# Performance work log

Hardware: AMD Instinct MI355X
Metric: run time of the kernel (lower is better)

## Reference

```python
import jax, jax.numpy as jnp
import numpy as np

NUM_HEADS = 16
WINDOW = 128  # local-attention half-width used by the mask generator
NEG_INF = -1e9


def setup_inputs() -> dict:
    key = jax.random.key(0)
    ks = jax.random.split(key, 12)
    T, N, C = 2048, 2, 1024
    s = 1.0 / np.sqrt(C)
    inp = {
        "q": jax.random.normal(ks[0], (T, N, C), jnp.float32),
        "k": jax.random.normal(ks[1], (T, N, C), jnp.float32),
        "v": jax.random.normal(ks[2], (T, N, C), jnp.float32),
        # MultiHeadDispatch: separate q/k/v input projections + output projection (with bias)
        "Wq": jax.random.normal(ks[3], (C, C), jnp.float32) * s,
        "bq": jnp.zeros((C,), jnp.float32),
        "Wk": jax.random.normal(ks[4], (C, C), jnp.float32) * s,
        "bk": jnp.zeros((C,), jnp.float32),
        "Wv": jax.random.normal(ks[5], (C, C), jnp.float32) * s,
        "bv": jnp.zeros((C,), jnp.float32),
        "Wo": jax.random.normal(ks[6], (C, C), jnp.float32) * s,
        "bo": jnp.zeros((C,), jnp.float32),
        "key_length": jax.random.randint(ks[7], (N,), 1, T, dtype=jnp.int32),
    }
    return inp


def _build_mask(Lq, Lk, key_length):
    # mask_generator: banded local-window mask, True = attend
    i = jnp.arange(Lq)[:, None]
    j = jnp.arange(Lk)[None, :]
    local = jnp.abs(i - j) <= WINDOW                      # (Lq, Lk)
    # forward(): mask[i, :, :key_length[i]] = 1  -> unmask prefix keys per batch elem
    prefix = j[None, :, :] < key_length[:, None, None]    # (N, Lq, Lk)
    return local[None, :, :] | prefix                     # (N, Lq, Lk) bool


def reference(q, k, v, Wq, bq, Wk, bk, Wv, bv, Wo, bo, key_length):
    T, N, C = q.shape
    H = NUM_HEADS
    Dh = C // H
    mask = _build_mask(q.shape[0], k.shape[0], key_length)  # (N, Lq, Lk)

    def heads(x, W, b):
        # (T, N, C) -> project -> (N, H, T, Dh)
        y = x @ W.T + b
        return jnp.transpose(y.reshape(x.shape[0], N, H, Dh), (1, 2, 0, 3))

    qh = heads(q, Wq, bq)
    kh = heads(k, Wk, bk)
    vh = heads(v, Wv, bv)

    scale = 1.0 / np.sqrt(Dh).astype(np.float32)
    scores = jnp.einsum('nhqd,nhkd->nhqk', qh, kh) * scale  # (N, H, Lq, Lk)
    scores = jnp.where(mask[:, None, :, :], scores, NEG_INF)
    att = jax.nn.softmax(scores, axis=-1)
    y = jnp.einsum('nhqk,nhkd->nhqd', att, vh)              # (N, H, Lq, Dh)
    y = jnp.transpose(y, (2, 0, 1, 3)).reshape(T, N, C)     # back to (t, n, c)
    return y @ Wo.T + bo
```

## Files before the change

### kernel.cpp

```cpp
#include <hip/hip_runtime.h>
#include <math.h>

#define T_DIM 2048
#define N_B   2
#define C_DIM 1024
#define H_DIM 16
#define DH    64
#define M_DIM 4096
#define WIN   128

typedef _Float16 h8 __attribute__((ext_vector_type(8)));
typedef float    f4 __attribute__((ext_vector_type(4)));

#if __has_builtin(__builtin_amdgcn_exp2f)
#define EXP2(x) __builtin_amdgcn_exp2f(x)
#else
#define EXP2(x) __expf((x) * 0.693147180559945f)
#endif

__device__ __forceinline__ void glds16(const _Float16* g, _Float16* l) {
    typedef const __attribute__((address_space(1))) unsigned int guint;
    typedef __attribute__((address_space(3))) unsigned int luint;
    __builtin_amdgcn_global_load_lds((guint*)g, (luint*)l, 16, 0, 0);
}

struct CvtA { const float* s; _Float16* d; int n; };
struct Cvt7 { CvtA a[7]; };

__global__ __launch_bounds__(256) void cvt_k(Cvt7 c) {
    CvtA A = c.a[blockIdx.y];
    const int i = (blockIdx.x * 256 + threadIdx.x) * 8;
    if (i >= A.n) return;
    const float4 v0 = *(const float4*)&A.s[i];
    const float4 v1 = *(const float4*)&A.s[i + 4];
    h8 o;
    o[0] = (_Float16)v0.x; o[1] = (_Float16)v0.y;
    o[2] = (_Float16)v0.z; o[3] = (_Float16)v0.w;
    o[4] = (_Float16)v1.x; o[5] = (_Float16)v1.y;
    o[6] = (_Float16)v1.z; o[7] = (_Float16)v1.w;
    *(h8*)&A.d[i] = o;
}

struct QkvArgs {
    const _Float16* x[3];
    const _Float16* w[3];
    const float*    b[3];
    _Float16*       out[3];
};

__global__ __launch_bounds__(256) void proj_qkv(QkvArgs args) {
    const int z = blockIdx.z;
    const _Float16* __restrict__ A = args.x[z];
    const _Float16* __restrict__ B = args.w[z];
    const float* __restrict__ bias = args.b[z];
    _Float16* __restrict__ out     = args.out[z];

    __shared__ _Float16 Asm[3][128 * 32];
    __shared__ _Float16 Bsm[3][128 * 32];
    const int tid  = threadIdx.x;
    const int lane = tid & 63;
    const int wave = tid >> 6;
    const int wr = wave >> 1, wc = wave & 1;
    const int l15 = lane & 15, hi = lane >> 4;
    const int m0 = blockIdx.x << 7;
    const int o0 = blockIdx.y << 7;

    auto STAGE = [&](int b, int k0) {
#pragma unroll
        for (int c = 0; c < 2; ++c) {
            const int chunk = tid + c * 256;
            const int row = chunk >> 2, c4 = chunk & 3;
            const int sc = (c4 ^ ((row >> 1) & 3)) << 3;
            glds16(&A[(size_t)(m0 + row) * C_DIM + k0 + sc], &Asm[b][chunk << 3]);
            glds16(&B[(size_t)(o0 + row) * C_DIM + k0 + sc], &Bsm[b][chunk << 3]);
        }
    };

    f4 acc[4][4];
    const f4 z4 = {0.f, 0.f, 0.f, 0.f};
#pragma unroll
    for (int i = 0; i < 4; ++i)
#pragma unroll
        for (int j = 0; j < 4; ++j) acc[i][j] = z4;

    STAGE(0, 0);
    STAGE(1, 32);
    int buf = 0;
    for (int k0 = 0; k0 < C_DIM; k0 += 32) {
        if (k0 + 32 < C_DIM) {
            asm volatile("s_waitcnt vmcnt(4)" ::: "memory");
        } else {
            asm volatile("s_waitcnt vmcnt(0)" ::: "memory");
        }
        __builtin_amdgcn_s_barrier();
        __builtin_amdgcn_sched_barrier(0);
        if (k0 + 64 < C_DIM) {
            const int nb = (buf + 2 >= 3) ? buf - 1 : buf + 2;
            STAGE(nb, k0 + 64);
        }

        h8 a[4], b[4];
#pragma unroll
        for (int mr = 0; mr < 4; ++mr) {
            const int R = wr * 64 + mr * 16 + l15;
            a[mr] = *(const h8*)&Asm[buf][R * 32 + ((hi ^ ((R >> 1) & 3)) << 3)];
        }
#pragma unroll
        for (int nf = 0; nf < 4; ++nf) {
            const int R = wc * 64 + nf * 16 + l15;
            b[nf] = *(const h8*)&Bsm[buf][R * 32 + ((hi ^ ((R >> 1) & 3)) << 3)];
        }
#pragma unroll
        for (int mr = 0; mr < 4; ++mr)
#pragma unroll
            for (int nf = 0; nf < 4; ++nf)
                acc[mr][nf] = __builtin_amdgcn_mfma_f32_16x16x32_f16(
                    a[mr], b[nf], acc[mr][nf], 0, 0, 0);

        buf = (buf + 1 >= 3) ? 0 : buf + 1;
    }

#pragma unroll
    for (int nf = 0; nf < 4; ++nf) {
        const int o = o0 + wc * 64 + nf * 16 + l15;
        const float bb = bias[o];
        const int hh = o >> 6, d = o & 63;
#pragma unroll
        for (int mr = 0; mr < 4; ++mr)
#pragma unroll
            for (int reg = 0; reg < 4; ++reg) {
                const int m = m0 + wr * 64 + mr * 16 + 4 * hi + reg;
                const float val = acc[mr][nf][reg] + bb;
                const int t = m >> 1, n = m & 1;
                if (z == 2) {
                    out[(((size_t)(n * H_DIM + hh)) * DH + d) * T_DIM + t] = (_Float16)val;
                } else {
                    out[(((size_t)(n * H_DIM + hh)) * T_DIM + t) * DH + d] = (_Float16)val;
                }
            }
    }
}

__global__ __launch_bounds__(256) void proj_o(
    const _Float16* __restrict__ A, const _Float16* __restrict__ B,
    const float* __restrict__ bias, float* __restrict__ out)
{
    __shared__ _Float16 Asm[3][128 * 32];
    __shared__ _Float16 Bsm[3][128 * 32];
    const int tid  = threadIdx.x;
    const int lane = tid & 63;
    const int wave = tid >> 6;
    const int wr = wave >> 1, wc = wave & 1;
    const int l15 = lane & 15, hi = lane >> 4;
    const int m0 = blockIdx.x << 7;
    const int o0 = blockIdx.y << 7;

    auto STAGE = [&](int b, int k0) {
#pragma unroll
        for (int c = 0; c < 2; ++c) {
            const int chunk = tid + c * 256;
            const int row = chunk >> 2, c4 = chunk & 3;
            const int sc = (c4 ^ ((row >> 1) & 3)) << 3;
            glds16(&A[(size_t)(m0 + row) * C_DIM + k0 + sc], &Asm[b][chunk << 3]);
            glds16(&B[(size_t)(o0 + row) * C_DIM + k0 + sc], &Bsm[b][chunk << 3]);
        }
    };

    f4 acc[4][4];
    const f4 z4 = {0.f, 0.f, 0.f, 0.f};
#pragma unroll
    for (int i = 0; i < 4; ++i)
#pragma unroll
        for (int j = 0; j < 4; ++j) acc[i][j] = z4;

    STAGE(0, 0);
    STAGE(1, 32);
    int buf = 0;
    for (int k0 = 0; k0 < C_DIM; k0 += 32) {
        if (k0 + 32 < C_DIM) {
            asm volatile("s_waitcnt vmcnt(4)" ::: "memory");
        } else {
            asm volatile("s_waitcnt vmcnt(0)" ::: "memory");
        }
        __builtin_amdgcn_s_barrier();
        __builtin_amdgcn_sched_barrier(0);
        if (k0 + 64 < C_DIM) {
            const int nb = (buf + 2 >= 3) ? buf - 1 : buf + 2;
            STAGE(nb, k0 + 64);
        }

        h8 a[4], b[4];
#pragma unroll
        for (int mr = 0; mr < 4; ++mr) {
            const int R = wr * 64 + mr * 16 + l15;
            a[mr] = *(const h8*)&Asm[buf][R * 32 + ((hi ^ ((R >> 1) & 3)) << 3)];
        }
#pragma unroll
        for (int nf = 0; nf < 4; ++nf) {
            const int R = wc * 64 + nf * 16 + l15;
            b[nf] = *(const h8*)&Bsm[buf][R * 32 + ((hi ^ ((R >> 1) & 3)) << 3)];
        }
#pragma unroll
        for (int mr = 0; mr < 4; ++mr)
#pragma unroll
            for (int nf = 0; nf < 4; ++nf)
                acc[mr][nf] = __builtin_amdgcn_mfma_f32_16x16x32_f16(
                    a[mr], b[nf], acc[mr][nf], 0, 0, 0);

        buf = (buf + 1 >= 3) ? 0 : buf + 1;
    }

#pragma unroll
    for (int nf = 0; nf < 4; ++nf) {
        const int o = o0 + wc * 64 + nf * 16 + l15;
        const float bb = bias[o];
#pragma unroll
        for (int mr = 0; mr < 4; ++mr)
#pragma unroll
            for (int reg = 0; reg < 4; ++reg) {
                const int m = m0 + wr * 64 + mr * 16 + 4 * hi + reg;
                out[(size_t)m * C_DIM + o] = acc[mr][nf][reg] + bb;
            }
    }
}

__global__ __launch_bounds__(256, 2) void attn_v7(
    const _Float16* __restrict__ QH, const _Float16* __restrict__ KH,
    const _Float16* __restrict__ VT, const int* __restrict__ key_length,
    _Float16* __restrict__ Y)
{
    __shared__ _Float16 Ks[2][64 * 64];
    __shared__ _Float16 Vs[2][64 * 64];
    __shared__ _Float16 Ps[4][32 * 72];

    const int nh = blockIdx.x;
    const int n  = nh >> 4;
    const int h  = nh & 15;
    const int qb = blockIdx.y << 7;
    const int kl = key_length[n];
    const int tid  = threadIdx.x;
    const int wave = tid >> 6;
    const int lane = tid & 63;
    const int l15 = lane & 15, hi = lane >> 4;
    const int qw = qb + wave * 32;
    const int swz = l15 & 7;

    const size_t hb = (size_t)nh * T_DIM * DH;
    const _Float16* Qb = QH + hb;
    const _Float16* Kb = KH + hb;
    const _Float16* Vb = VT + hb;

    const int klc0 = ((kl + 63) >> 6) << 6;
    const int klc  = (klc0 < T_DIM) ? klc0 : T_DIM;
    const int blo  = (qb >= WIN) ? ((qb - WIN) & ~63) : 0;
    int bhi = ((qb + 127 + WIN) >> 6) << 6;
    if (bhi > T_DIM - 64) bhi = T_DIM - 64;
    auto nxt = [&](int k0) -> int {
        k0 += 64;
        if (k0 < klc) return k0;
        if (k0 < blo) k0 = blo;
        return (k0 <= bhi) ? k0 : -1;
    };

    auto STAGE = [&](int b, int k0) {
#pragma unroll
        for (int c = 0; c < 2; ++c) {
            const int slot = wave * 128 + c * 64 + lane;
            const int r = slot >> 3, c16 = slot & 7;
            const int sc = (c16 ^ (r & 7)) << 3;
            glds16(&Kb[(size_t)(k0 + r) * DH + sc], &Ks[b][slot << 3]);
        }
#pragma unroll
        for (int c = 0; c < 2; ++c) {
            const int slot = wave * 128 + c * 64 + lane;
            const int r = slot >> 3, c16 = slot & 7;
            const int sc = (c16 ^ (r & 7)) << 3;
            glds16(&Vb[(size_t)r * T_DIM + k0 + sc], &Vs[b][slot << 3]);
        }
    };

    h8 qa[2][2];
#pragma unroll
    for (int mr = 0; mr < 2; ++mr)
#pragma unroll
        for (int ks = 0; ks < 2; ++ks)
            qa[mr][ks] = *(const h8*)&Qb[(size_t)(qw + mr * 16 + l15) * DH + ks * 32 + hi * 8];

    f4 O[2][4];
    const f4 z4 = {0.f, 0.f, 0.f, 0.f};
#pragma unroll
    for (int mr = 0; mr < 2; ++mr)
#pragma unroll
        for (int df = 0; df < 4; ++df) O[mr][df] = z4;
    float m_i[2][4], lp[2][4];
#pragma unroll
    for (int mr = 0; mr < 2; ++mr)
#pragma unroll
        for (int r = 0; r < 4; ++r) { m_i[mr][r] = -1e30f; lp[mr][r] = 0.f; }

    const float SC = 0.18033688f;

    auto TILE = [&](int b, int k0) {
        h8 kb[2][4];
#pragma unroll
        for (int ks = 0; ks < 2; ++ks)
#pragma unroll
            for (int cf = 0; cf < 4; ++cf)
                kb[ks][cf] = *(const h8*)&Ks[b][(cf * 16 + l15) * 64 +
                                                (((ks * 4 + hi) ^ swz) << 3)];

        f4 sacc[2][4];
#pragma unroll
        for (int mr = 0; mr < 2; ++mr)
#pragma unroll
            for (int cf = 0; cf < 4; ++cf) sacc[mr][cf] = z4;
#pragma unroll
        for (int ks = 0; ks < 2; ++ks)
#pragma unroll
            for (int mr = 0; mr < 2; ++mr)
#pragma unroll
                for (int cf = 0; cf < 4; ++cf)
                    sacc[mr][cf] = __builtin_amdgcn_mfma_f32_16x16x32_f16(
                        qa[mr][ks], kb[ks][cf], sacc[mr][cf], 0, 0, 0);

        h8 vb[2][4];
#pragma unroll
        for (int ks = 0; ks < 2; ++ks)
#pragma unroll
            for (int df = 0; df < 4; ++df)
                vb[ks][df] = *(const h8*)&Vs[b][(df * 16 + l15) * 64 +
                                                (((ks * 4 + hi) ^ swz) << 3)];

        const bool full = (k0 + 63 < kl) ||
                          (k0 >= qw + 31 - WIN && k0 + 63 <= qw + WIN);

#pragma unroll
        for (int mr = 0; mr < 2; ++mr) {
            if (full) {
#pragma unroll
                for (int cf = 0; cf < 4; ++cf)
#pragma unroll
                    for (int reg = 0; reg < 4; ++reg)
                        sacc[mr][cf][reg] *= SC;
            } else {
#pragma unroll
                for (int cf = 0; cf < 4; ++cf)
#pragma unroll
                    for (int reg = 0; reg < 4; ++reg) {
                        const int i = qw + mr * 16 + 4 * hi + reg;
                        const int j = k0 + cf * 16 + l15;
                        const int dd = i - j;
                        const bool ok = (dd <= WIN && dd >= -WIN) || (j < kl);
                        sacc[mr][cf][reg] = ok ? sacc[mr][cf][reg] * SC : -1e9f;
                    }
            }
        }

        float lm[2][4];
        bool need = false;
#pragma unroll
        for (int mr = 0; mr < 2; ++mr)
#pragma unroll
            for (int reg = 0; reg < 4; ++reg) {
                lm[mr][reg] = fmaxf(fmaxf(sacc[mr][0][reg], sacc[mr][1][reg]),
                                    fmaxf(sacc[mr][2][reg], sacc[mr][3][reg]));
                need = need || (lm[mr][reg] > m_i[mr][reg]);
            }
        if (__any(need)) {
#pragma unroll
            for (int mr = 0; mr < 2; ++mr)
#pragma unroll
                for (int reg = 0; reg < 4; ++reg) {
                    float mt = lm[mr][reg];
                    mt = fmaxf(mt, __shfl_xor(mt, 1));
                    mt = fmaxf(mt, __shfl_xor(mt, 2));
                    mt = fmaxf(mt, __shfl_xor(mt, 4));
                    mt = fmaxf(mt, __shfl_xor(mt, 8));
                    const float mnew = fmaxf(m_i[mr][reg], mt + 3.0f);
                    const float rr = EXP2(m_i[mr][reg] - mnew);
                    m_i[mr][reg] = mnew;
                    lp[mr][reg] *= rr;
#pragma unroll
                    for (int df = 0; df < 4; ++df) O[mr][df][reg] *= rr;
                }
        }

        _Float16* Pw = &Ps[wave][0];
#pragma unroll
        for (int mr = 0; mr < 2; ++mr)
#pragma unroll
            for (int reg = 0; reg < 4; ++reg) {
                const int row = mr * 16 + 4 * hi + reg;
                const float mi = m_i[mr][reg];
                float acc = 0.f;
#pragma unroll
                for (int cf = 0; cf < 4; ++cf) {
                    const float p = EXP2(sacc[mr][cf][reg] - mi);
                    acc += p;
                    Pw[row * 72 + cf * 16 + l15] = (_Float16)p;
                }
                lp[mr][reg] += acc;
            }

        h8 pa[2][2];
#pragma unroll
        for (int mr = 0; mr < 2; ++mr)
#pragma unroll
            for (int ks = 0; ks < 2; ++ks)
                pa[mr][ks] = *(const h8*)&Pw[(mr * 16 + l15) * 72 + ks * 32 + hi * 8];
#pragma unroll
        for (int ks = 0; ks < 2; ++ks)
#pragma unroll
            for (int mr = 0; mr < 2; ++mr)
#pragma unroll
                for (int df = 0; df < 4; ++df)
                    O[mr][df] = __builtin_amdgcn_mfma_f32_16x16x32_f16(
                        pa[mr][ks], vb[ks][df], O[mr][df], 0, 0, 0);
    };

    STAGE(0, 0);
    __syncthreads();
    int buf = 0, k0 = 0, k1 = nxt(0);
    for (;;) {
        if (k1 >= 0) STAGE(buf ^ 1, k1);
        const bool wkeep = (k0 < kl) || (k0 <= qw + 31 + WIN && k0 + 63 >= qw - WIN);
        if (wkeep) TILE(buf, k0);
        __syncthreads();
        if (k1 < 0) break;
        k0 = k1; k1 = nxt(k0); buf ^= 1;
    }

    float lf[2][4];
#pragma unroll
    for (int mr = 0; mr < 2; ++mr)
#pragma unroll
        for (int reg = 0; reg < 4; ++reg) {
            float l = lp[mr][reg];
            l += __shfl_xor(l, 1); l += __shfl_xor(l, 2);
            l += __shfl_xor(l, 4); l += __shfl_xor(l, 8);
            lf[mr][reg] = l;
        }

#pragma unroll
    for (int mr = 0; mr < 2; ++mr)
#pragma unroll
        for (int reg = 0; reg < 4; ++reg) {
            const float inv = 1.f / lf[mr][reg];
            const int i = qw + mr * 16 + 4 * hi + reg;
#pragma unroll
            for (int df = 0; df < 4; ++df) {
                Y[((size_t)i * N_B + n) * C_DIM + h * DH + df * 16 + l15] =
                    (_Float16)(O[mr][df][reg] * inv);
            }
        }
}

extern "C" void kernel_launch(void* const* d_in, const int* in_sizes, int n_in,
                              void* d_out, int out_size, void* d_ws, size_t ws_size,
                              hipStream_t stream) {
    const float* q  = (const float*)d_in[0];
    const float* k  = (const float*)d_in[1];
    const float* v  = (const float*)d_in[2];
    const float* Wq = (const float*)d_in[3];
    const float* bq = (const float*)d_in[4];
    const float* Wk = (const float*)d_in[5];
    const float* bk = (const float*)d_in[6];
    const float* Wv = (const float*)d_in[7];
    const float* bv = (const float*)d_in[8];
    const float* Wo = (const float*)d_in[9];
    const float* bo = (const float*)d_in[10];
    const int*   kl = (const int*)d_in[11];

    const int NX = M_DIM * C_DIM;
    const int NW = C_DIM * C_DIM;

    _Float16* xq = (_Float16*)d_ws;
    _Float16* xk = xq + NX;
    _Float16* xv = xk + NX;
    _Float16* wq = xv + NX;
    _Float16* wk = wq + NW;
    _Float16* wv = wk + NW;
    _Float16* wo = wv + NW;
    _Float16* QHh = wo + NW;
    _Float16* KHh = QHh + NX;
    _Float16* VTh = KHh + NX;
    _Float16* Yh  = xq;

    Cvt7 c;
    c.a[0] = {q,  xq, NX}; c.a[1] = {k,  xk, NX}; c.a[2] = {v,  xv, NX};
    c.a[3] = {Wq, wq, NW}; c.a[4] = {Wk, wk, NW};
    c.a[5] = {Wv, wv, NW}; c.a[6] = {Wo, wo, NW};
    cvt_k<<<dim3(NX / (256 * 8), 7), 256, 0, stream>>>(c);

    QkvArgs qa;
    qa.x[0] = xq; qa.x[1] = xk; qa.x[2] = xv;
    qa.w[0] = wq; qa.w[1] = wk; qa.w[2] = wv;
    qa.b[0] = bq; qa.b[1] = bk; qa.b[2] = bv;
    qa.out[0] = QHh; qa.out[1] = KHh; qa.out[2] = VTh;
    proj_qkv<<<dim3(M_DIM / 128, C_DIM / 128, 3), 256, 0, stream>>>(qa);

    attn_v7<<<dim3(N_B * H_DIM, T_DIM / 128), 256, 0, stream>>>(QHh, KHh, VTh, kl, Yh);

    proj_o<<<dim3(M_DIM / 128, C_DIM / 128), 256, 0, stream>>>(Yh, wo, bo, (float*)d_out);
}
```

Measured before the change: 113.3 us.

## Halve GEMM M-tile to 64 and stage epilogue through LDS for vector stores

Both projection GEMMs now use a 64x128 output tile instead of 128x128, which doubles the number of blocks so more of the GPU's compute units are busy. The A and B tiles now live in one combined shared buffer. The epilogue writes results into LDS first, then each wave stores them with 16-byte vectorized global writes. This replaces the scattered scalar stores into the head-major and transposed V layouts. The cost is less operand reuse per block, since B is loaded twice as often, plus an extra LDS round trip and barrier in the epilogue.

```diff
diff --git a/kernel.cpp b/kernel.cpp
--- a/kernel.cpp
+++ b/kernel.cpp
@@ -55,31 +55,38 @@
     const float* __restrict__ bias = args.b[z];
     _Float16* __restrict__ out     = args.out[z];
 
-    __shared__ _Float16 Asm[3][128 * 32];
-    __shared__ _Float16 Bsm[3][128 * 32];
+    __shared__ _Float16 Sm[3][6144];
+    _Float16* smf = &Sm[0][0];
+
     const int tid  = threadIdx.x;
     const int lane = tid & 63;
     const int wave = tid >> 6;
     const int wr = wave >> 1, wc = wave & 1;
     const int l15 = lane & 15, hi = lane >> 4;
-    const int m0 = blockIdx.x << 7;
+    const int m0 = blockIdx.x << 6;
     const int o0 = blockIdx.y << 7;
 
     auto STAGE = [&](int b, int k0) {
+        {
+            const int chunk = tid;
+            const int row = chunk >> 2, c4 = chunk & 3;
+            const int sc = (c4 ^ ((row >> 1) & 3)) << 3;
+            glds16(&A[(size_t)(m0 + row) * C_DIM + k0 + sc], &Sm[b][chunk << 3]);
+        }
 #pragma unroll
         for (int c = 0; c < 2; ++c) {
             const int chunk = tid + c * 256;
             const int row = chunk >> 2, c4 = chunk & 3;
             const int sc = (c4 ^ ((row >> 1) & 3)) << 3;
-            glds16(&A[(size_t)(m0 + row) * C_DIM + k0 + sc], &Asm[b][chunk << 3]);
-            glds16(&B[(size_t)(o0 + row) * C_DIM + k0 + sc], &Bsm[b][chunk << 3]);
+            glds16(&B[(size_t)(o0 + row) * C_DIM + k0 + sc],
+                   &Sm[b][2048 + (chunk << 3)]);
         }
     };
 
-    f4 acc[4][4];
+    f4 acc[2][4];
     const f4 z4 = {0.f, 0.f, 0.f, 0.f};
 #pragma unroll
-    for (int i = 0; i < 4; ++i)
+    for (int i = 0; i < 2; ++i)
 #pragma unroll
         for (int j = 0; j < 4; ++j) acc[i][j] = z4;
 
@@ -88,7 +95,7 @@
     int buf = 0;
     for (int k0 = 0; k0 < C_DIM; k0 += 32) {
         if (k0 + 32 < C_DIM) {
-            asm volatile("s_waitcnt vmcnt(4)" ::: "memory");
+            asm volatile("s_waitcnt vmcnt(3)" ::: "memory");
         } else {
             asm volatile("s_waitcnt vmcnt(0)" ::: "memory");
         }
@@ -99,19 +106,19 @@
             STAGE(nb, k0 + 64);
         }
 
-        h8 a[4], b[4];
-#pragma unroll
-        for (int mr = 0; mr < 4; ++mr) {
-            const int R = wr * 64 + mr * 16 + l15;
-            a[mr] = *(const h8*)&Asm[buf][R * 32 + ((hi ^ ((R >> 1) & 3)) << 3)];
+        h8 a[2], b[4];
+#pragma unroll
+        for (int mr = 0; mr < 2; ++mr) {
+            const int R = wr * 32 + mr * 16 + l15;
+            a[mr] = *(const h8*)&Sm[buf][R * 32 + ((hi ^ ((R >> 1) & 3)) << 3)];
         }
 #pragma unroll
         for (int nf = 0; nf < 4; ++nf) {
             const int R = wc * 64 + nf * 16 + l15;
-            b[nf] = *(const h8*)&Bsm[buf][R * 32 + ((hi ^ ((R >> 1) & 3)) << 3)];
-        }
-#pragma unroll
-        for (int mr = 0; mr < 4; ++mr)
+            b[nf] = *(const h8*)&Sm[buf][2048 + R * 32 + ((hi ^ ((R >> 1) & 3)) << 3)];
+        }
+#pragma unroll
+        for (int mr = 0; mr < 2; ++mr)
 #pragma unroll
             for (int nf = 0; nf < 4; ++nf)
                 acc[mr][nf] = __builtin_amdgcn_mfma_f32_16x16x32_f16(
@@ -120,24 +127,56 @@
         buf = (buf + 1 >= 3) ? 0 : buf + 1;
     }
 
-#pragma unroll
-    for (int nf = 0; nf < 4; ++nf) {
-        const int o = o0 + wc * 64 + nf * 16 + l15;
-        const float bb = bias[o];
-        const int hh = o >> 6, d = o & 63;
-#pragma unroll
-        for (int mr = 0; mr < 4; ++mr)
-#pragma unroll
-            for (int reg = 0; reg < 4; ++reg) {
-                const int m = m0 + wr * 64 + mr * 16 + 4 * hi + reg;
-                const float val = acc[mr][nf][reg] + bb;
-                const int t = m >> 1, n = m & 1;
-                if (z == 2) {
-                    out[(((size_t)(n * H_DIM + hh)) * DH + d) * T_DIM + t] = (_Float16)val;
-                } else {
-                    out[(((size_t)(n * H_DIM + hh)) * T_DIM + t) * DH + d] = (_Float16)val;
+    __syncthreads();
+    const int hh = (o0 >> 6) + wc;
+    if (z == 2) {
+        _Float16* ws = smf + wave * 3072;
+#pragma unroll
+        for (int nf = 0; nf < 4; ++nf) {
+            const float bb = bias[o0 + wc * 64 + nf * 16 + l15];
+            const int d = nf * 16 + l15;
+#pragma unroll
+            for (int mr = 0; mr < 2; ++mr)
+#pragma unroll
+                for (int reg = 0; reg < 4; ++reg) {
+                    const int ml = mr * 16 + 4 * hi + reg;
+                    ws[((ml & 1) * 64 + d) * 24 + (ml >> 1)] =
+                        (_Float16)(acc[mr][nf][reg] + bb);
                 }
-            }
+        }
+        const int tbase = (m0 + wr * 32) >> 1;
+#pragma unroll
+        for (int it = 0; it < 4; ++it) {
+            const int c = lane + it * 64;
+            const int rowi = c >> 1;
+            const int th = (c & 1) << 3;
+            const h8 v = *(const h8*)&ws[rowi * 24 + th];
+            const int n = rowi >> 6, d = rowi & 63;
+            *(h8*)&out[((size_t)((n * 16 + hh) * 64 + d)) * T_DIM + tbase + th] = v;
+        }
+    } else {
+        _Float16* ws = smf + wave * 2304;
+#pragma unroll
+        for (int nf = 0; nf < 4; ++nf) {
+            const float bb = bias[o0 + wc * 64 + nf * 16 + l15];
+#pragma unroll
+            for (int mr = 0; mr < 2; ++mr)
+#pragma unroll
+                for (int reg = 0; reg < 4; ++reg)
+                    ws[(mr * 16 + 4 * hi + reg) * 72 + nf * 16 + l15] =
+                        (_Float16)(acc[mr][nf][reg] + bb);
+        }
+        const int t0 = (m0 + wr * 32) >> 1;
+#pragma unroll
+        for (int it = 0; it < 4; ++it) {
+            const int c = lane + it * 64;
+            const int nn = c >> 7;
+            const int tq = (c >> 3) & 15;
+            const int d8 = (c & 7) << 3;
+            const int ml = (tq << 1) | nn;
+            const h8 v = *(const h8*)&ws[ml * 72 + d8];
+            *(h8*)&out[((size_t)(nn * 16 + hh) * T_DIM + t0 + tq) * DH + d8] = v;
+        }
     }
 }
 
@@ -145,31 +184,38 @@
     const _Float16* __restrict__ A, const _Float16* __restrict__ B,
     const float* __restrict__ bias, float* __restrict__ out)
 {
-    __shared__ _Float16 Asm[3][128 * 32];
-    __shared__ _Float16 Bsm[3][128 * 32];
+    __shared__ _Float16 Sm[3][6144];
+    _Float16* smf = &Sm[0][0];
+
     const int tid  = threadIdx.x;
     const int lane = tid & 63;
     const int wave = tid >> 6;
     const int wr = wave >> 1, wc = wave & 1;
     const int l15 = lane & 15, hi = lane >> 4;
-    const int m0 = blockIdx.x << 7;
+    const int m0 = blockIdx.x << 6;
     const int o0 = blockIdx.y << 7;
 
     auto STAGE = [&](int b, int k0) {
+        {
+            const int chunk = tid;
+            const int row = chunk >> 2, c4 = chunk & 3;
+            const int sc = (c4 ^ ((row >> 1) & 3)) << 3;
+            glds16(&A[(size_t)(m0 + row) * C_DIM + k0 + sc], &Sm[b][chunk << 3]);
+        }
 #pragma unroll
         for (int c = 0; c < 2; ++c) {
             const int chunk = tid + c * 256;
             const int row = chunk >> 2, c4 = chunk & 3;
             const int sc = (c4 ^ ((row >> 1) & 3)) << 3;
-            glds16(&A[(size_t)(m0 + row) * C_DIM + k0 + sc], &Asm[b][chunk << 3]);
-            glds16(&B[(size_t)(o0 + row) * C_DIM + k0 + sc], &Bsm[b][chunk << 3]);
+            glds16(&B[(size_t)(o0 + row) * C_DIM + k0 + sc],
+                   &Sm[b][2048 + (chunk << 3)]);
         }
     };
 
-    f4 acc[4][4];
+    f4 acc[2][4];
     const f4 z4 = {0.f, 0.f, 0.f, 0.f};
 #pragma unroll
-    for (int i = 0; i < 4; ++i)
+    for (int i = 0; i < 2; ++i)
 #pragma unroll
         for (int j = 0; j < 4; ++j) acc[i][j] = z4;
 
@@ -178,7 +224,7 @@
     int buf = 0;
     for (int k0 = 0; k0 < C_DIM; k0 += 32) {
         if (k0 + 32 < C_DIM) {
-            asm volatile("s_waitcnt vmcnt(4)" ::: "memory");
+            asm volatile("s_waitcnt vmcnt(3)" ::: "memory");
         } else {
             asm volatile("s_waitcnt vmcnt(0)" ::: "memory");
         }
@@ -189,19 +235,19 @@
             STAGE(nb, k0 + 64);
         }
 
-        h8 a[4], b[4];
-#pragma unroll
-        for (int mr = 0; mr < 4; ++mr) {
-            const int R = wr * 64 + mr * 16 + l15;
-            a[mr] = *(const h8*)&Asm[buf][R * 32 + ((hi ^ ((R >> 1) & 3)) << 3)];
+        h8 a[2], b[4];
+#pragma unroll
+        for (int mr = 0; mr < 2; ++mr) {
+            const int R = wr * 32 + mr * 16 + l15;
+            a[mr] = *(const h8*)&Sm[buf][R * 32 + ((hi ^ ((R >> 1) & 3)) << 3)];
         }
 #pragma unroll
         for (int nf = 0; nf < 4; ++nf) {
             const int R = wc * 64 + nf * 16 + l15;
-            b[nf] = *(const h8*)&Bsm[buf][R * 32 + ((hi ^ ((R >> 1) & 3)) << 3)];
-        }
-#pragma unroll
-        for (int mr = 0; mr < 4; ++mr)
+            b[nf] = *(const h8*)&Sm[buf][2048 + R * 32 + ((hi ^ ((R >> 1) & 3)) << 3)];
+        }
+#pragma unroll
+        for (int mr = 0; mr < 2; ++mr)
 #pragma unroll
             for (int nf = 0; nf < 4; ++nf)
                 acc[mr][nf] = __builtin_amdgcn_mfma_f32_16x16x32_f16(
@@ -210,17 +256,25 @@
         buf = (buf + 1 >= 3) ? 0 : buf + 1;
     }
 
+    __syncthreads();
+    float* wsf = (float*)smf + wave * 2176;
 #pragma unroll
     for (int nf = 0; nf < 4; ++nf) {
-        const int o = o0 + wc * 64 + nf * 16 + l15;
-        const float bb = bias[o];
-#pragma unroll
-        for (int mr = 0; mr < 4; ++mr)
-#pragma unroll
-            for (int reg = 0; reg < 4; ++reg) {
-                const int m = m0 + wr * 64 + mr * 16 + 4 * hi + reg;
-                out[(size_t)m * C_DIM + o] = acc[mr][nf][reg] + bb;
-            }
+        const float bb = bias[o0 + wc * 64 + nf * 16 + l15];
+#pragma unroll
+        for (int mr = 0; mr < 2; ++mr)
+#pragma unroll
+            for (int reg = 0; reg < 4; ++reg)
+                wsf[(mr * 16 + 4 * hi + reg) * 68 + nf * 16 + l15] =
+                    acc[mr][nf][reg] + bb;
+    }
+#pragma unroll
+    for (int it = 0; it < 8; ++it) {
+        const int c = lane + it * 64;
+        const int ml = c >> 4;
+        const int o4 = (c & 15) << 2;
+        const f4 v = *(const f4*)&wsf[ml * 68 + o4];
+        *(f4*)&out[(size_t)(m0 + wr * 32 + ml) * C_DIM + o0 + wc * 64 + o4] = v;
     }
 }
 
@@ -497,9 +551,9 @@
     qa.w[0] = wq; qa.w[1] = wk; qa.w[2] = wv;
     qa.b[0] = bq; qa.b[1] = bk; qa.b[2] = bv;
     qa.out[0] = QHh; qa.out[1] = KHh; qa.out[2] = VTh;
-    proj_qkv<<<dim3(M_DIM / 128, C_DIM / 128, 3), 256, 0, stream>>>(qa);
+    proj_qkv<<<dim3(M_DIM / 64, C_DIM / 128, 3), 256, 0, stream>>>(qa);
 
     attn_v7<<<dim3(N_B * H_DIM, T_DIM / 128), 256, 0, stream>>>(QHh, KHh, VTh, kl, Yh);
 
-    proj_o<<<dim3(M_DIM / 128, C_DIM / 128), 256, 0, stream>>>(Yh, wo, bo, (float*)d_out);
+    proj_o<<<dim3(M_DIM / 64, C_DIM / 128), 256, 0, stream>>>(Yh, wo, bo, (float*)d_out);
 }
```

Result: faster. 110.0 us (-3.0%).
